# Kernel optimization log

Hardware: AMD Instinct MI355X
Metric: run time of the kernel (lower is better)

The kernel has to match this reference:

```python
import jax, jax.numpy as jnp
import numpy as np

B, C, H, W = 4, 64, 256, 512


def setup_inputs() -> dict:
    key = jax.random.key(0)
    k1, k2 = jax.random.split(key)
    input1 = jax.random.normal(k1, (B, C, H, W), dtype=jnp.float32)
    # horizontal displacement field (pixels)
    input2 = jax.random.normal(k2, (B, 1, H, W), dtype=jnp.float32)
    return {"input1": input1, "input2": input2}


def reference(input1, input2):
    # 1D (along-width) bilinear resampling: out[b,c,h,w] = input1 sampled at x = w + disp[b,h,w]
    b, c, h, w = input1.shape
    disp = input2[:, 0]                                   # [B,H,W]
    x = jnp.arange(w, dtype=input1.dtype) + disp          # sample coords [B,H,W]
    valid = ((x >= 0) & (x <= w - 1)).astype(input1.dtype)
    x0 = jnp.floor(x)
    frac = x - x0                                         # bilinear weight
    i0 = jnp.clip(x0, 0, w - 1).astype(jnp.int32)
    i1 = jnp.clip(x0 + 1, 0, w - 1).astype(jnp.int32)
    idx0 = jnp.broadcast_to(i0[:, None], (b, c, h, w))
    idx1 = jnp.broadcast_to(i1[:, None], (b, c, h, w))
    g0 = jnp.take_along_axis(input1, idx0, axis=3)
    g1 = jnp.take_along_axis(input1, idx1, axis=3)
    out = ((1.0 - frac)[:, None] * g0 + frac[:, None] * g1) * valid[:, None]
    return out
```

## Files before the change

### kernel.cpp

```cpp
#include <hip/hip_runtime.h>


#define B 4
#define C 64
#define H 256
#define W 512
#define CCHUNK 8

__global__ __launch_bounds__(256) void resample1d_kernel(
    const float* __restrict__ in1,
    const float* __restrict__ in2,
    float* __restrict__ out)
{
    const int HW = H * W;
    int idx = blockIdx.x * 256 + threadIdx.x;
    int b  = idx / HW;
    int hw = idx - b * HW;
    int w  = hw & (W - 1);
    int c0 = blockIdx.y * CCHUNK;

    float disp = in2[idx];
    float x = (float)w + disp;
    bool valid = (x >= 0.0f) && (x <= (float)(W - 1));
    float x0 = floorf(x);
    float frac = x - x0;

    float x0c = fminf(fmaxf(x0,        0.0f), (float)(W - 1));
    float x1c = fminf(fmaxf(x0 + 1.0f, 0.0f), (float)(W - 1));
    int i0 = (int)x0c;
    int i1 = (int)x1c;
    float w0 = valid ? (1.0f - frac) : 0.0f;
    float w1 = valid ? frac : 0.0f;

    const float* rowbase = in1 + (size_t)b * C * HW + (size_t)c0 * HW + (size_t)(hw - w);
    float*       outp    = out + (size_t)b * C * HW + (size_t)c0 * HW + (size_t)hw;

    float g0[CCHUNK], g1[CCHUNK];
    #pragma unroll
    for (int c = 0; c < CCHUNK; ++c) {
        g0[c] = rowbase[(size_t)c * HW + i0];
        g1[c] = rowbase[(size_t)c * HW + i1];
    }
    #pragma unroll
    for (int c = 0; c < CCHUNK; ++c) {
        float r = w0 * g0[c] + w1 * g1[c];
        __builtin_nontemporal_store(r, &outp[(size_t)c * HW]);
    }
}

extern "C" void kernel_launch(void* const* d_in, const int* in_sizes, int n_in,
                              void* d_out, int out_size, void* d_ws, size_t ws_size,
                              hipStream_t stream) {
    const float* in1 = (const float*)d_in[0];
    const float* in2 = (const float*)d_in[1];
    float* out = (float*)d_out;

    int pixels = B * H * W;
    dim3 grid(pixels / 256, C / CCHUNK), block(256);
    resample1d_kernel<<<grid, block, 0, stream>>>(in1, in2, out);
}
```

Before: 50.40 us.

## Stage input rows in per-wave LDS and gather from shared memory

Each block now handles one (b,h) row. Every wavefront loads a full 512-wide input row per channel into its own LDS buffer with coalesced float4 loads, then does the bilinear gather from LDS. Sample indices and weights are computed once per pixel and reused across 8 channels, and the next channel's row is prefetched into registers while the current one is gathered. This replaces scattered global gathers with streaming loads. It relies on wave-synchronous LDS access with no barrier, and it lowers the number of blocks in the grid.

```diff
diff --git a/kernel.cpp b/kernel.cpp
--- a/kernel.cpp
+++ b/kernel.cpp
@@ -5,46 +5,67 @@
 #define C 64
 #define H 256
 #define W 512
-#define CCHUNK 8
+#define WAVES 4
+#define CPW 8
 
 __global__ __launch_bounds__(256) void resample1d_kernel(
     const float* __restrict__ in1,
     const float* __restrict__ in2,
     float* __restrict__ out)
 {
-    const int HW = H * W;
-    int idx = blockIdx.x * 256 + threadIdx.x;
-    int b  = idx / HW;
-    int hw = idx - b * HW;
-    int w  = hw & (W - 1);
-    int c0 = blockIdx.y * CCHUNK;
+    __shared__ float rowbuf[WAVES][W];
 
-    float disp = in2[idx];
-    float x = (float)w + disp;
-    bool valid = (x >= 0.0f) && (x <= (float)(W - 1));
-    float x0 = floorf(x);
-    float frac = x - x0;
+    const int tid  = threadIdx.x;
+    const int wid  = tid >> 6;
+    const int lane = tid & 63;
 
-    float x0c = fminf(fmaxf(x0,        0.0f), (float)(W - 1));
-    float x1c = fminf(fmaxf(x0 + 1.0f, 0.0f), (float)(W - 1));
-    int i0 = (int)x0c;
-    int i1 = (int)x1c;
-    float w0 = valid ? (1.0f - frac) : 0.0f;
-    float w1 = valid ? frac : 0.0f;
+    const int bh = blockIdx.x;
+    const int b  = bh >> 8;
+    const int h  = bh & (H - 1);
+    const int cbase = blockIdx.y * (WAVES * CPW) + wid * CPW;
 
-    const float* rowbase = in1 + (size_t)b * C * HW + (size_t)c0 * HW + (size_t)(hw - w);
-    float*       outp    = out + (size_t)b * C * HW + (size_t)c0 * HW + (size_t)hw;
+    const float* disp_row = in2 + (size_t)bh * W;
+    int   i0[8], i1[8];
+    float w0[8], w1[8];
+    #pragma unroll
+    for (int p = 0; p < 8; ++p) {
+        int w = lane + 64 * p;
+        float x = (float)w + disp_row[w];
+        bool valid = (x >= 0.0f) && (x <= (float)(W - 1));
+        float x0 = floorf(x);
+        float frac = x - x0;
+        float x0c = fminf(fmaxf(x0, 0.0f), (float)(W - 1));
+        i0[p] = (int)x0c;
+        i1[p] = min(i0[p] + 1, W - 1);
+        w0[p] = valid ? (1.0f - frac) : 0.0f;
+        w1[p] = valid ? frac : 0.0f;
+    }
 
-    float g0[CCHUNK], g1[CCHUNK];
+    float* rb = rowbuf[wid];
+
+    const size_t chan_stride = (size_t)H * W;
+    const float* src = in1 + ((size_t)b * C + cbase) * chan_stride + (size_t)h * W;
+    float*       dst = out + ((size_t)b * C + cbase) * chan_stride + (size_t)h * W;
+
+    float4 r0 = *(const float4*)(src + 4 * lane);
+    float4 r1 = *(const float4*)(src + 256 + 4 * lane);
+
     #pragma unroll
-    for (int c = 0; c < CCHUNK; ++c) {
-        g0[c] = rowbase[(size_t)c * HW + i0];
-        g1[c] = rowbase[(size_t)c * HW + i1];
-    }
-    #pragma unroll
-    for (int c = 0; c < CCHUNK; ++c) {
-        float r = w0 * g0[c] + w1 * g1[c];
-        __builtin_nontemporal_store(r, &outp[(size_t)c * HW]);
+    for (int cc = 0; cc < CPW; ++cc) {
+        *(float4*)(rb + 4 * lane)       = r0;
+        *(float4*)(rb + 256 + 4 * lane) = r1;
+        if (cc + 1 < CPW) {
+            const float* s2 = src + (size_t)(cc + 1) * chan_stride;
+            r0 = *(const float4*)(s2 + 4 * lane);
+            r1 = *(const float4*)(s2 + 256 + 4 * lane);
+        }
+        float* d = dst + (size_t)cc * chan_stride;
+        #pragma unroll
+        for (int p = 0; p < 8; ++p) {
+            float g0 = rb[i0[p]];
+            float g1 = rb[i1[p]];
+            __builtin_nontemporal_store(w0[p] * g0 + w1[p] * g1, d + lane + 64 * p);
+        }
     }
 }
 
@@ -55,7 +76,6 @@
     const float* in2 = (const float*)d_in[1];
     float* out = (float*)d_out;
 
-    int pixels = B * H * W;
-    dim3 grid(pixels / 256, C / CCHUNK), block(256);
+    dim3 grid(B * H, C / (WAVES * CPW)), block(WAVES * 64);
     resample1d_kernel<<<grid, block, 0, stream>>>(in1, in2, out);
 }
```

New measurement: 47.86 us. -5.0%, faster.
